# Optimization experiments

Measured on AMD Instinct MI355X. Metric: run time of the kernel, lower is better.

The kernel has to match this reference:

```python
import jax, jax.numpy as jnp
import numpy as np
import math

HEAD_SIZE = 64
N_EMBED = 1024
BLOCK_SIZE = 2048
BATCH = 8


def setup_inputs() -> dict:
    key = jax.random.key(0)
    k1, k2, k3, k4, k5 = jax.random.split(key, 5)
    index = jax.random.normal(k1, (BATCH, BLOCK_SIZE, N_EMBED), dtype=jnp.float32)
    memory = jax.random.normal(k2, (BATCH, BLOCK_SIZE, N_EMBED), dtype=jnp.float32)
    # torch Linear weights: [out_features, in_features], kaiming-uniform-ish init
    bound = 1.0 / math.sqrt(N_EMBED)
    Wq = jax.random.uniform(k3, (HEAD_SIZE, N_EMBED), jnp.float32, -bound, bound)
    Wk = jax.random.uniform(k4, (HEAD_SIZE, N_EMBED), jnp.float32, -bound, bound)
    Wv = jax.random.uniform(k5, (HEAD_SIZE, N_EMBED), jnp.float32, -bound, bound)
    return {"index": index, "memory": memory, "Wq": Wq, "Wk": Wk, "Wv": Wv}


def reference(index, memory, Wq, Wk, Wv):
    # q/k/v projections (Linear without bias: x @ W.T)
    q = jnp.einsum('btc,hc->bth', index, Wq)   # [B,T,H]
    k = jnp.einsum('bsc,hc->bsh', memory, Wk)  # [B,S,H]
    v = jnp.einsum('bsc,hc->bsh', memory, Wv)  # [B,S,H]
    scale = 1.0 / math.sqrt(HEAD_SIZE)
    w = jnp.einsum('bth,bsh->bts', q, k) * scale  # [B,T,S]
    # causal mask: tril==0 -> -inf
    T = index.shape[1]
    causal = jnp.tril(jnp.ones((BLOCK_SIZE, BLOCK_SIZE), dtype=bool))[:T, :T]
    w = jnp.where(causal, w, -jnp.inf)
    w = jax.nn.softmax(w, axis=-1)
    out = jnp.einsum('bts,bsh->bth', w, v)  # [B,T,H]
    return out
```

## Files before the change

### kernel.cpp

```cpp
#include <hip/hip_runtime.h>
#include <math.h>

typedef __bf16 bf16;
typedef __bf16 bf16x4 __attribute__((ext_vector_type(4)));
typedef __bf16 bf16x8 __attribute__((ext_vector_type(8)));
typedef float f32x4 __attribute__((ext_vector_type(4)));

#define MFMA16(a,b,c) __builtin_amdgcn_mfma_f32_16x16x32_bf16((a),(b),(c),0,0,0)

static constexpr int HS  = 64;
static constexpr int SEQ = 2048;
static constexpr int NE  = 1024;
static constexpr int NB  = 8;

__device__ __forceinline__ bf16x8 cvt8(float4 a, float4 b) {
  bf16x8 r;
  r[0]=(bf16)a.x; r[1]=(bf16)a.y; r[2]=(bf16)a.z; r[3]=(bf16)a.w;
  r[4]=(bf16)b.x; r[5]=(bf16)b.y; r[6]=(bf16)b.z; r[7]=(bf16)b.w;
  return r;
}

__device__ __forceinline__ void gload16(const void* g, void* l) {
  __builtin_amdgcn_global_load_lds(
      (const __attribute__((address_space(1))) void*)g,
      (__attribute__((address_space(3))) void*)l, 16, 0, 0);
}

__global__ __launch_bounds__(256) void wcvt_kernel(
    const float* __restrict__ Wq, const float* __restrict__ Wk,
    const float* __restrict__ Wv, bf16* __restrict__ wqb,
    bf16* __restrict__ wkb, bf16* __restrict__ wvb)
{
  int i = (blockIdx.x * 256 + threadIdx.x) * 4;
  float4 q = *(const float4*)(Wq + i);
  float4 k = *(const float4*)(Wk + i);
  float4 v = *(const float4*)(Wv + i);
  bf16x4 qo, ko, vo;
  qo[0]=(bf16)(q.x*0.125f); qo[1]=(bf16)(q.y*0.125f); qo[2]=(bf16)(q.z*0.125f); qo[3]=(bf16)(q.w*0.125f);
  ko[0]=(bf16)k.x; ko[1]=(bf16)k.y; ko[2]=(bf16)k.z; ko[3]=(bf16)k.w;
  vo[0]=(bf16)v.x; vo[1]=(bf16)v.y; vo[2]=(bf16)v.z; vo[3]=(bf16)v.w;
  *(bf16x4*)(wqb + i) = qo;
  *(bf16x4*)(wkb + i) = ko;
  *(bf16x4*)(wvb + i) = vo;
}

template<int KV>
__device__ __forceinline__ void proj_body(
    const float* __restrict__ X, const bf16* __restrict__ W0,
    const bf16* __restrict__ W1, bf16* __restrict__ out0,
    bf16* __restrict__ outVT, int slab, char* smem)
{
  const int tid  = threadIdx.x;
  const int lane = tid & 63;
  const int w    = tid >> 6;
  const int m    = lane & 15;
  const int g    = lane >> 4;
  const int rowBase = slab * 64;

  char* Xb  = smem;
  char* W0b = smem + 32768;
  char* W1b = smem + 49152;

  const f32x4 vz = {0.f,0.f,0.f,0.f};
  f32x4 accA[4] = {vz, vz, vz, vz};
  f32x4 accB[4] = {vz, vz, vz, vz};

  const float* Xbase = X + (size_t)rowBase * NE;

  auto stage = [&](int kt, int buf) {
#pragma unroll
    for (int q = 0; q < 4; ++q) {
      int r = (q*4 + w)*4 + (lane >> 4);
      int s = lane & 15;
      const float* src = Xbase + (size_t)r * NE + kt*64 + ((s ^ (r & 15)) * 4);
      void* dst = Xb + buf*16384 + (q*4 + w)*1024;
      gload16(src, dst);
    }
#pragma unroll
    for (int q = 0; q < 2; ++q) {
      int r = (q*4 + w)*8 + (lane >> 3);
      int s = lane & 7;
      size_t soff = (size_t)r * NE + kt*64 + ((s ^ (r & 7)) * 8);
      void* dst0 = W0b + buf*8192 + (q*4 + w)*1024;
      gload16(W0 + soff, dst0);
      if (KV) {
        void* dst1 = W1b + buf*8192 + (q*4 + w)*1024;
        gload16(W1 + soff, dst1);
      }
    }
  };

  auto compute = [&](int buf) {
#pragma unroll
    for (int kk = 0; kk < 2; ++kk) {
      const int arow = 16*w + m;
      const int s0 = 2*(kk*4 + g);
      const char* ab = Xb + buf*16384 + arow*256;
      float4 x0 = *(const float4*)(ab + (( s0      ^ (arow & 15)) * 16));
      float4 x1 = *(const float4*)(ab + (((s0 + 1) ^ (arow & 15)) * 16));
      bf16x8 af = cvt8(x0, x1);
#pragma unroll
      for (int n = 0; n < 4; ++n) {
        const int col = 16*n + m;
        const int ws  = kk*4 + g;
        bf16x8 b0 = *(const bf16x8*)(W0b + buf*8192 + col*128 + ((ws ^ (col & 7)) * 16));
        accA[n] = MFMA16(af, b0, accA[n]);
        if (KV) {
          bf16x8 b1 = *(const bf16x8*)(W1b + buf*8192 + col*128 + ((ws ^ (col & 7)) * 16));
          accB[n] = MFMA16(af, b1, accB[n]);
        }
      }
    }
  };

  stage(0, 0);
  __syncthreads();
  int buf = 0;
  for (int kt = 0; kt < 16; ++kt) {
    if (kt + 1 < 16) stage(kt + 1, buf ^ 1);
    compute(buf);
    __syncthreads();
    buf ^= 1;
  }

#pragma unroll
  for (int n = 0; n < 4; ++n)
#pragma unroll
    for (int i = 0; i < 4; ++i) {
      int row = rowBase + 16*w + 4*g + i;
      int h   = 16*n + m;
      out0[(size_t)row * HS + h] = (bf16)accA[n][i];
      if (KV)
        outVT[((size_t)(row >> 11) * HS + h) * SEQ + (row & 2047)] =
            (bf16)accB[n][i];
    }
}

__global__ __launch_bounds__(256, 2) void proj_kernel(
    const float* __restrict__ index, const float* __restrict__ memory,
    const bf16* __restrict__ wqb, const bf16* __restrict__ wkb,
    const bf16* __restrict__ wvb, bf16* __restrict__ qb,
    bf16* __restrict__ kb, bf16* __restrict__ vtb)
{
  __shared__ __align__(1024) char smem[65536];
  if (blockIdx.x < 256)
    proj_body<0>(index,  wqb, nullptr, qb, nullptr, blockIdx.x, smem);
  else
    proj_body<1>(memory, wkb, wvb,     kb, vtb, blockIdx.x - 256, smem);
}

__global__ __launch_bounds__(128, 2) void attn_kernel(
    const bf16* __restrict__ qb, const bf16* __restrict__ kb,
    const bf16* __restrict__ vtb, float* __restrict__ out)
{
  __shared__ __align__(16) bf16 Ks[2][64][72];
  __shared__ __align__(16) bf16 VTs[2][64][72];
  __shared__ __align__(16) bf16 Ps[2][16][72];

  const int tid  = threadIdx.x;
  const int lane = tid & 63;
  const int w    = tid >> 6;
  const int m    = lane & 15;
  const int g    = lane >> 4;
  const int qt   = 127 - blockIdx.x;
  const int b    = blockIdx.y;
  const int nkv  = (qt >> 2) + 1;
  const int r0   = lane >> 1;
  const int hh   = (lane & 1) * 32;

  bf16x8 qf0 = *(const bf16x8*)(qb + ((size_t)b*SEQ + qt*16 + m)*HS + g*8);
  bf16x8 qf1 = *(const bf16x8*)(qb + ((size_t)b*SEQ + qt*16 + m)*HS + 32 + g*8);

  const f32x4 vz = {0.f,0.f,0.f,0.f};
  f32x4 o_acc[4] = {vz, vz, vz, vz};
  float mrun[4], lrun[4];
#pragma unroll
  for (int i = 0; i < 4; ++i) { mrun[i] = -INFINITY; lrun[i] = 0.f; }

  bf16x8 kp[8], vp[8];
  const bf16* kbB = kb  + (size_t)b*SEQ*HS;
  const bf16* vtB = vtb + (size_t)b*HS*SEQ;

  auto loadKV = [&](int j) {
    const bf16* kt_ = kbB + (size_t)j*64*HS;
    const bf16* vt_ = vtB + j*64;
#pragma unroll
    for (int q = 0; q < 4; ++q) {
      kp[q]   = *(const bf16x8*)(kt_ + (size_t)r0*64        + hh + q*8);
      kp[4+q] = *(const bf16x8*)(kt_ + (size_t)(r0+32)*64   + hh + q*8);
      vp[q]   = *(const bf16x8*)(vt_ + (size_t)r0*SEQ       + hh + q*8);
      vp[4+q] = *(const bf16x8*)(vt_ + (size_t)(r0+32)*SEQ  + hh + q*8);
    }
  };
  auto writeKV = [&]() {
#pragma unroll
    for (int q = 0; q < 4; ++q) {
      *(bf16x8*)&Ks[w][r0][hh + q*8]      = kp[q];
      *(bf16x8*)&Ks[w][r0+32][hh + q*8]   = kp[4+q];
      *(bf16x8*)&VTs[w][r0][hh + q*8]     = vp[q];
      *(bf16x8*)&VTs[w][r0+32][hh + q*8]  = vp[4+q];
    }
  };

  int j = w;
  if (j < nkv) {
    loadKV(j);
    writeKV();
    while (true) {
      const int jn = j + 2;
      const bool more = jn < nkv;
      if (more) loadKV(jn);

      f32x4 s_acc[4];
#pragma unroll
      for (int n = 0; n < 4; ++n) {
        f32x4 z = vz;
        z = MFMA16(qf0, *(const bf16x8*)&Ks[w][16*n + m][g*8], z);
        z = MFMA16(qf1, *(const bf16x8*)&Ks[w][16*n + m][32 + g*8], z);
        s_acc[n] = z;
      }
      if (j == nkv - 1) {
#pragma unroll
        for (int n = 0; n < 4; ++n) {
          int gk = j*64 + 16*n + m;
#pragma unroll
          for (int i = 0; i < 4; ++i)
            if (gk > qt*16 + 4*g + i) s_acc[n][i] = -INFINITY;
        }
      }

      float corr[4], tsum[4];
#pragma unroll
      for (int i = 0; i < 4; ++i) {
        float mx = fmaxf(fmaxf(s_acc[0][i], s_acc[1][i]),
                         fmaxf(s_acc[2][i], s_acc[3][i]));
        mx = fmaxf(mx, __shfl_xor(mx, 1));
        mx = fmaxf(mx, __shfl_xor(mx, 2));
        mx = fmaxf(mx, __shfl_xor(mx, 4));
        mx = fmaxf(mx, __shfl_xor(mx, 8));
        float mnew = fmaxf(mrun[i], mx);
        corr[i] = __expf(mrun[i] - mnew);
        mrun[i] = mnew;
        tsum[i] = 0.f;
      }
#pragma unroll
      for (int n = 0; n < 4; ++n)
#pragma unroll
        for (int i = 0; i < 4; ++i) {
          float p = __expf(s_acc[n][i] - mrun[i]);
          tsum[i] += p;
          Ps[w][4*g + i][16*n + m] = (bf16)p;
        }
#pragma unroll
      for (int i = 0; i < 4; ++i) {
        float s = tsum[i];
        s += __shfl_xor(s, 1);
        s += __shfl_xor(s, 2);
        s += __shfl_xor(s, 4);
        s += __shfl_xor(s, 8);
        lrun[i] = lrun[i] * corr[i] + s;
      }
#pragma unroll
      for (int n = 0; n < 4; ++n)
#pragma unroll
        for (int i = 0; i < 4; ++i) o_acc[n][i] *= corr[i];

#pragma unroll
      for (int kk = 0; kk < 2; ++kk) {
        bf16x8 pf = *(const bf16x8*)&Ps[w][m][kk*32 + g*8];
#pragma unroll
        for (int n = 0; n < 4; ++n) {
          bf16x8 vf = *(const bf16x8*)&VTs[w][16*n + m][kk*32 + g*8];
          o_acc[n] = MFMA16(pf, vf, o_acc[n]);
        }
      }

      if (!more) break;
      writeKV();
      j = jn;
    }
  }

  float* PO = (float*)&Ks[w][0][0];
  float* PM = (float*)&VTs[w][0][0];
#pragma unroll
  for (int n = 0; n < 4; ++n)
#pragma unroll
    for (int i = 0; i < 4; ++i)
      PO[(4*g + i)*64 + 16*n + m] = o_acc[n][i];
  if (m == 0) {
#pragma unroll
    for (int i = 0; i < 4; ++i) {
      PM[4*g + i]      = mrun[i];
      PM[16 + 4*g + i] = lrun[i];
    }
  }
  __syncthreads();

  {
    const int r  = tid >> 3;
    const int c0 = (tid & 7) * 8;
    const float* O0 = (const float*)&Ks[0][0][0];
    const float* O1 = (const float*)&Ks[1][0][0];
    const float* M0 = (const float*)&VTs[0][0][0];
    const float* M1 = (const float*)&VTs[1][0][0];
    float m0 = M0[r], l0 = M0[16 + r];
    float m1 = M1[r], l1 = M1[16 + r];
    float mx = fmaxf(m0, m1);
    float s0 = __expf(m0 - mx), s1 = __expf(m1 - mx);
    float inv = 1.f / (s0*l0 + s1*l1);
    float4 x0 = *(const float4*)(O0 + r*64 + c0);
    float4 x1 = *(const float4*)(O0 + r*64 + c0 + 4);
    float4 y0 = *(const float4*)(O1 + r*64 + c0);
    float4 y1 = *(const float4*)(O1 + r*64 + c0 + 4);
    float4 o0, o1;
    o0.x=(x0.x*s0+y0.x*s1)*inv; o0.y=(x0.y*s0+y0.y*s1)*inv;
    o0.z=(x0.z*s0+y0.z*s1)*inv; o0.w=(x0.w*s0+y0.w*s1)*inv;
    o1.x=(x1.x*s0+y1.x*s1)*inv; o1.y=(x1.y*s0+y1.y*s1)*inv;
    o1.z=(x1.z*s0+y1.z*s1)*inv; o1.w=(x1.w*s0+y1.w*s1)*inv;
    float* op = out + ((size_t)b*SEQ + qt*16 + r) * HS + c0;
    *(float4*)(op)     = o0;
    *(float4*)(op + 4) = o1;
  }
}

extern "C" void kernel_launch(void* const* d_in, const int* in_sizes, int n_in,
                              void* d_out, int out_size, void* d_ws, size_t ws_size,
                              hipStream_t stream) {
  (void)in_sizes; (void)n_in; (void)out_size; (void)ws_size;
  const float* index  = (const float*)d_in[0];
  const float* memory = (const float*)d_in[1];
  const float* Wq     = (const float*)d_in[2];
  const float* Wk     = (const float*)d_in[3];
  const float* Wv     = (const float*)d_in[4];
  float* out = (float*)d_out;

  bf16* qb  = (bf16*)d_ws;
  bf16* kb  = qb  + (size_t)NB * SEQ * HS;
  bf16* vtb = kb  + (size_t)NB * SEQ * HS;
  bf16* wqb = vtb + (size_t)NB * SEQ * HS;
  bf16* wkb = wqb + (size_t)HS * NE;
  bf16* wvb = wkb + (size_t)HS * NE;

  wcvt_kernel<<<dim3(64), 256, 0, stream>>>(Wq, Wk, Wv, wqb, wkb, wvb);
  proj_kernel<<<dim3(512), 256, 0, stream>>>(index, memory, wqb, wkb, wvb, qb, kb, vtb);
  attn_kernel<<<dim3(128, 8), 128, 0, stream>>>(qb, kb, vtb, out);
}
```

Before: 81.22 us.

## Triple-buffer projection loads and transpose attention MFMAs to keep softmax per-lane

Result: faster. 72.37 us (-10.9%).

```diff
diff --git a/kernel.cpp b/kernel.cpp
--- a/kernel.cpp
+++ b/kernel.cpp
@@ -58,8 +58,8 @@
   const int rowBase = slab * 64;
 
   char* Xb  = smem;
-  char* W0b = smem + 32768;
-  char* W1b = smem + 49152;
+  char* W0b = smem + 49152;
+  char* W1b = smem + 73728;
 
   const f32x4 vz = {0.f,0.f,0.f,0.f};
   f32x4 accA[4] = {vz, vz, vz, vz};
@@ -114,13 +114,20 @@
   };
 
   stage(0, 0);
-  __syncthreads();
-  int buf = 0;
-  for (int kt = 0; kt < 16; ++kt) {
-    if (kt + 1 < 16) stage(kt + 1, buf ^ 1);
-    compute(buf);
-    __syncthreads();
-    buf ^= 1;
+  stage(1, 1);
+#pragma unroll
+  for (int t = 0; t < 16; ++t) {
+    if (t < 15) {
+      if (KV) asm volatile("s_waitcnt vmcnt(8)" ::: "memory");
+      else    asm volatile("s_waitcnt vmcnt(6)" ::: "memory");
+    } else {
+      asm volatile("s_waitcnt vmcnt(0)" ::: "memory");
+    }
+    __builtin_amdgcn_s_barrier();
+    __builtin_amdgcn_sched_barrier(0);
+    if (t + 2 < 16) stage(t + 2, (t + 2) % 3);
+    __builtin_amdgcn_sched_barrier(0);
+    compute(t % 3);
   }
 
 #pragma unroll
@@ -142,14 +149,14 @@
     const bf16* __restrict__ wvb, bf16* __restrict__ qb,
     bf16* __restrict__ kb, bf16* __restrict__ vtb)
 {
-  __shared__ __align__(1024) char smem[65536];
+  __shared__ __align__(1024) char smem[98304];
   if (blockIdx.x < 256)
     proj_body<0>(index,  wqb, nullptr, qb, nullptr, blockIdx.x, smem);
   else
     proj_body<1>(memory, wkb, wvb,     kb, vtb, blockIdx.x - 256, smem);
 }
 
-__global__ __launch_bounds__(128, 2) void attn_kernel(
+__global__ __launch_bounds__(128) void attn_kernel(
     const bf16* __restrict__ qb, const bf16* __restrict__ kb,
     const bf16* __restrict__ vtb, float* __restrict__ out)
 {
@@ -173,9 +180,7 @@
 
   const f32x4 vz = {0.f,0.f,0.f,0.f};
   f32x4 o_acc[4] = {vz, vz, vz, vz};
-  float mrun[4], lrun[4];
-#pragma unroll
-  for (int i = 0; i < 4; ++i) { mrun[i] = -INFINITY; lrun[i] = 0.f; }
+  float mrun = -INFINITY, lrun = 0.f;
 
   bf16x8 kp[8], vp[8];
   const bf16* kbB = kb  + (size_t)b*SEQ*HS;
@@ -213,66 +218,57 @@
 
       f32x4 s_acc[4];
 #pragma unroll
-      for (int n = 0; n < 4; ++n) {
+      for (int na = 0; na < 4; ++na) {
         f32x4 z = vz;
-        z = MFMA16(qf0, *(const bf16x8*)&Ks[w][16*n + m][g*8], z);
-        z = MFMA16(qf1, *(const bf16x8*)&Ks[w][16*n + m][32 + g*8], z);
-        s_acc[n] = z;
+        z = MFMA16(*(const bf16x8*)&Ks[w][16*na + m][g*8],      qf0, z);
+        z = MFMA16(*(const bf16x8*)&Ks[w][16*na + m][32 + g*8], qf1, z);
+        s_acc[na] = z;
       }
       if (j == nkv - 1) {
-#pragma unroll
-        for (int n = 0; n < 4; ++n) {
-          int gk = j*64 + 16*n + m;
+        const int q_ = qt*16 + m;
+#pragma unroll
+        for (int na = 0; na < 4; ++na)
 #pragma unroll
           for (int i = 0; i < 4; ++i)
-            if (gk > qt*16 + 4*g + i) s_acc[n][i] = -INFINITY;
+            if (j*64 + 16*na + 4*g + i > q_) s_acc[na][i] = -INFINITY;
+      }
+
+      float mx = fmaxf(
+        fmaxf(fmaxf(fmaxf(s_acc[0][0],s_acc[0][1]),fmaxf(s_acc[0][2],s_acc[0][3])),
+              fmaxf(fmaxf(s_acc[1][0],s_acc[1][1]),fmaxf(s_acc[1][2],s_acc[1][3]))),
+        fmaxf(fmaxf(fmaxf(s_acc[2][0],s_acc[2][1]),fmaxf(s_acc[2][2],s_acc[2][3])),
+              fmaxf(fmaxf(s_acc[3][0],s_acc[3][1]),fmaxf(s_acc[3][2],s_acc[3][3]))));
+      mx = fmaxf(mx, __shfl_xor(mx, 16));
+      mx = fmaxf(mx, __shfl_xor(mx, 32));
+      float mnew = fmaxf(mrun, mx);
+      float corr = __expf(mrun - mnew);
+      mrun = mnew;
+      float ts = 0.f;
+#pragma unroll
+      for (int na = 0; na < 4; ++na) {
+        bf16x4 pk;
+#pragma unroll
+        for (int i = 0; i < 4; ++i) {
+          float p = __expf(s_acc[na][i] - mnew);
+          ts += p;
+          pk[i] = (bf16)p;
         }
-      }
-
-      float corr[4], tsum[4];
-#pragma unroll
-      for (int i = 0; i < 4; ++i) {
-        float mx = fmaxf(fmaxf(s_acc[0][i], s_acc[1][i]),
-                         fmaxf(s_acc[2][i], s_acc[3][i]));
-        mx = fmaxf(mx, __shfl_xor(mx, 1));
-        mx = fmaxf(mx, __shfl_xor(mx, 2));
-        mx = fmaxf(mx, __shfl_xor(mx, 4));
-        mx = fmaxf(mx, __shfl_xor(mx, 8));
-        float mnew = fmaxf(mrun[i], mx);
-        corr[i] = __expf(mrun[i] - mnew);
-        mrun[i] = mnew;
-        tsum[i] = 0.f;
-      }
-#pragma unroll
-      for (int n = 0; n < 4; ++n)
-#pragma unroll
-        for (int i = 0; i < 4; ++i) {
-          float p = __expf(s_acc[n][i] - mrun[i]);
-          tsum[i] += p;
-          Ps[w][4*g + i][16*n + m] = (bf16)p;
-        }
-#pragma unroll
-      for (int i = 0; i < 4; ++i) {
-        float s = tsum[i];
-        s += __shfl_xor(s, 1);
-        s += __shfl_xor(s, 2);
-        s += __shfl_xor(s, 4);
-        s += __shfl_xor(s, 8);
-        lrun[i] = lrun[i] * corr[i] + s;
-      }
-#pragma unroll
-      for (int n = 0; n < 4; ++n)
-#pragma unroll
-        for (int i = 0; i < 4; ++i) o_acc[n][i] *= corr[i];
-
-#pragma unroll
-      for (int kk = 0; kk < 2; ++kk) {
-        bf16x8 pf = *(const bf16x8*)&Ps[w][m][kk*32 + g*8];
-#pragma unroll
-        for (int n = 0; n < 4; ++n) {
-          bf16x8 vf = *(const bf16x8*)&VTs[w][16*n + m][kk*32 + g*8];
-          o_acc[n] = MFMA16(pf, vf, o_acc[n]);
-        }
+        *(bf16x4*)&Ps[w][m][16*na + 4*g] = pk;
+      }
+      ts += __shfl_xor(ts, 16);
+      ts += __shfl_xor(ts, 32);
+      lrun = lrun * corr + ts;
+#pragma unroll
+      for (int nd = 0; nd < 4; ++nd)
+#pragma unroll
+        for (int i = 0; i < 4; ++i) o_acc[nd][i] *= corr;
+
+      bf16x8 pf0 = *(const bf16x8*)&Ps[w][m][g*8];
+      bf16x8 pf1 = *(const bf16x8*)&Ps[w][m][32 + g*8];
+#pragma unroll
+      for (int nd = 0; nd < 4; ++nd) {
+        o_acc[nd] = MFMA16(*(const bf16x8*)&VTs[w][16*nd + m][g*8],      pf0, o_acc[nd]);
+        o_acc[nd] = MFMA16(*(const bf16x8*)&VTs[w][16*nd + m][32 + g*8], pf1, o_acc[nd]);
       }
 
       if (!more) break;
@@ -284,17 +280,9 @@
   float* PO = (float*)&Ks[w][0][0];
   float* PM = (float*)&VTs[w][0][0];
 #pragma unroll
-  for (int n = 0; n < 4; ++n)
-#pragma unroll
-    for (int i = 0; i < 4; ++i)
-      PO[(4*g + i)*64 + 16*n + m] = o_acc[n][i];
-  if (m == 0) {
-#pragma unroll
-    for (int i = 0; i < 4; ++i) {
-      PM[4*g + i]      = mrun[i];
-      PM[16 + 4*g + i] = lrun[i];
-    }
-  }
+  for (int nd = 0; nd < 4; ++nd)
+    *(f32x4*)&PO[m*68 + 16*nd + 4*g] = o_acc[nd];
+  if (g == 0) { PM[m] = mrun; PM[16 + m] = lrun; }
   __syncthreads();
 
   {
@@ -309,10 +297,10 @@
     float mx = fmaxf(m0, m1);
     float s0 = __expf(m0 - mx), s1 = __expf(m1 - mx);
     float inv = 1.f / (s0*l0 + s1*l1);
-    float4 x0 = *(const float4*)(O0 + r*64 + c0);
-    float4 x1 = *(const float4*)(O0 + r*64 + c0 + 4);
-    float4 y0 = *(const float4*)(O1 + r*64 + c0);
-    float4 y1 = *(const float4*)(O1 + r*64 + c0 + 4);
+    float4 x0 = *(const float4*)(O0 + r*68 + c0);
+    float4 x1 = *(const float4*)(O0 + r*68 + c0 + 4);
+    float4 y0 = *(const float4*)(O1 + r*68 + c0);
+    float4 y1 = *(const float4*)(O1 + r*68 + c0 + 4);
     float4 o0, o1;
     o0.x=(x0.x*s0+y0.x*s1)*inv; o0.y=(x0.y*s0+y0.y*s1)*inv;
     o0.z=(x0.z*s0+y0.z*s1)*inv; o0.w=(x0.w*s0+y0.w*s1)*inv;
```
